# Kernel optimization log

Hardware: AMD Instinct MI355X
Metric: run time of the kernel (lower is better)

The kernel has to match this reference:

```python
import jax, jax.numpy as jnp
import numpy as np

N = 100_000          # ent_num
D = 256              # ent_dim
E_RAND = 3_200_000   # random edges (avg degree 32); + N self loops
NEG_SLOPE = 0.2      # LeakyReLU slope used by SpGraphAttentionLayer


def setup_inputs() -> dict:
    key = jax.random.key(0)
    k0, k1, k2, k3, k4, k5 = jax.random.split(key, 6)
    edges_rand = jax.random.randint(k0, (2, E_RAND), 0, N, dtype=jnp.int32)
    self_loops = jnp.tile(jnp.arange(N, dtype=jnp.int32)[None, :], (2, 1))
    edges = jnp.concatenate([edges_rand, self_loops], axis=1)  # [2, E]
    scale_w = 1.0 / np.sqrt(D).astype(np.float32)
    scale_a = 0.1 / np.sqrt(D).astype(np.float32)
    emb = jax.random.normal(k1, (N, D), jnp.float32)
    W1 = jax.random.normal(k2, (D, D), jnp.float32) * scale_w
    a1 = jax.random.normal(k3, (2 * D,), jnp.float32) * scale_a
    W2 = jax.random.normal(k4, (D, D), jnp.float32) * scale_w
    a2 = jax.random.normal(k5, (2 * D,), jnp.float32) * scale_a
    return {"emb": emb, "W1": W1, "a1": a1, "W2": W2, "a2": a2, "edges": edges}


def gat_layer(h, W, a, src, dst):
    # h: [N, D] node features; edges (src -> aggregates from dst)
    h2 = h @ W                              # [N, D]
    s_src = h2 @ a[:D]                      # [N] contribution of a . h_src
    s_dst = h2 @ a[D:]                      # [N] contribution of a . h_dst
    score = s_src[src] + s_dst[dst]         # [E] = a . [h_src; h_dst]
    e = jnp.exp(-jax.nn.leaky_relu(score, NEG_SLOPE))  # [E], pyGAT sparse form
    denom = jax.ops.segment_sum(e, src, num_segments=h.shape[0])          # [N]
    num = jax.ops.segment_sum(e[:, None] * h2[dst], src,
                              num_segments=h.shape[0])                    # [N, D]
    return jax.nn.elu(num / denom[:, None])


def reference(emb, W1, a1, W2, a2, edges):
    src, dst = edges[0], edges[1]
    h = gat_layer(emb, W1, a1, src, dst)
    h = gat_layer(h, W2, a2, src, dst)
    return h
```

## Files before the change

kernel.cpp:

```cpp
#include <hip/hip_runtime.h>
#include <hip/hip_bf16.h>

#define D 256
#define NEG_SLOPE 0.2f
#define BM 128
#define BN 128
#define BK 64
#define LDK 72
#define CAP 96

using bf16x8 = __attribute__((ext_vector_type(8))) __bf16;
using f32x4  = __attribute__((ext_vector_type(4))) float;
using u32x4  = __attribute__((ext_vector_type(4))) unsigned int;

__device__ __forceinline__ float bf2f(unsigned short u) {
    return __uint_as_float(((unsigned int)u) << 16);
}
__device__ __forceinline__ unsigned short f2bf(float f) {
    unsigned int u = __float_as_uint(f);
    unsigned int r = (u + 0x7FFF + ((u >> 16) & 1)) >> 16;
    return (unsigned short)r;
}


__global__ __launch_bounds__(256) void prep_kernel(
    const float* __restrict__ W1, const float* __restrict__ W2,
    unsigned short* __restrict__ WT1, unsigned short* __restrict__ WT2,
    int4* __restrict__ zbase, int nz16)
{
    const int b = blockIdx.x, tid = threadIdx.x;
    if (b < 256) {
        WT1[(size_t)tid * D + b] = f2bf(W1[(size_t)b * D + tid]);
    } else if (b < 512) {
        const int k = b - 256;
        WT2[(size_t)tid * D + k] = f2bf(W2[(size_t)k * D + tid]);
    } else {
        const int w = (b - 512) * 256 + tid;
        if (w < nz16) zbase[w] = make_int4(0, 0, 0, 0);
    }
}


__global__ void fill_kernel(const int* __restrict__ src, const int* __restrict__ dst,
                            int* __restrict__ fillp, int* __restrict__ col, int E) {
    int t = blockIdx.x * blockDim.x + threadIdx.x;
    if (t < E) {
        const int s = src[t];
        const int pos = atomicAdd(&fillp[s], 1);
        col[(size_t)s * CAP + pos] = dst[t];
    }
}


__global__ __launch_bounds__(256) void gemm_mfma(
    const unsigned short* __restrict__ Ab, const float* __restrict__ Af,
    const unsigned short* __restrict__ BT,
    unsigned short* __restrict__ C, int M,
    const float* __restrict__ av, float* __restrict__ s_src, float* __restrict__ s_dst)
{
    __shared__ unsigned short smem[2 * BM * LDK];
    unsigned short* As_ = smem;
    unsigned short* Bs_ = smem + BM * LDK;
    const int tid = threadIdx.x;
    const int m0 = blockIdx.x * BM;
    const int n0 = blockIdx.y * BN;
    const int lane = tid & 63;
    const int wv = tid >> 6;
    const int wm = (wv & 1) * 64;
    const int wn = (wv >> 1) * 64;
    const int l15 = lane & 15;
    const int quad = lane >> 4;

    f32x4 acc[4][4];
    #pragma unroll
    for (int i = 0; i < 4; ++i)
        #pragma unroll
        for (int j = 0; j < 4; ++j)
            acc[i][j] = (f32x4){0.f, 0.f, 0.f, 0.f};

    for (int k0 = 0; k0 < D; k0 += BK) {
        #pragma unroll
        for (int c = tid; c < BM * 8; c += 256) {
            const int row = c >> 3, j = c & 7;
            const int gr = m0 + row;
            uint4 avv = make_uint4(0, 0, 0, 0);
            if (gr < M) {
                if (Af) {
                    const float* p = Af + (size_t)gr * D + k0 + j * 8;
                    const float4 f0 = *(const float4*)p;
                    const float4 f1 = *(const float4*)(p + 4);
                    avv.x = (unsigned int)f2bf(f0.x) | ((unsigned int)f2bf(f0.y) << 16);
                    avv.y = (unsigned int)f2bf(f0.z) | ((unsigned int)f2bf(f0.w) << 16);
                    avv.z = (unsigned int)f2bf(f1.x) | ((unsigned int)f2bf(f1.y) << 16);
                    avv.w = (unsigned int)f2bf(f1.z) | ((unsigned int)f2bf(f1.w) << 16);
                } else {
                    avv = *(const uint4*)(Ab + (size_t)gr * D + k0 + j * 8);
                }
            }
            *(uint4*)(As_ + row * LDK + j * 8) = avv;
            const uint4 bv = *(const uint4*)(BT + (size_t)(n0 + row) * D + k0 + j * 8);
            *(uint4*)(Bs_ + row * LDK + j * 8) = bv;
        }
        __syncthreads();
        #pragma unroll
        for (int s = 0; s < 2; ++s) {
            bf16x8 af[4], bfr[4];
            #pragma unroll
            for (int i = 0; i < 4; ++i)
                af[i] = *(const bf16x8*)(As_ + (wm + i * 16 + l15) * LDK + s * 32 + quad * 8);
            #pragma unroll
            for (int j = 0; j < 4; ++j)
                bfr[j] = *(const bf16x8*)(Bs_ + (wn + j * 16 + l15) * LDK + s * 32 + quad * 8);
            #pragma unroll
            for (int i = 0; i < 4; ++i)
                #pragma unroll
                for (int j = 0; j < 4; ++j)
                    acc[i][j] = __builtin_amdgcn_mfma_f32_16x16x32_bf16(
                        af[i], bfr[j], acc[i][j], 0, 0, 0);
        }
        __syncthreads();
    }

    unsigned short* Cw = smem + wv * (64 * LDK);
    #pragma unroll
    for (int i = 0; i < 4; ++i)
        #pragma unroll
        for (int j = 0; j < 4; ++j)
            #pragma unroll
            for (int r = 0; r < 4; ++r)
                Cw[(i * 16 + quad * 4 + r) * LDK + j * 16 + l15] = f2bf(acc[i][j][r]);
    __syncthreads();
    const int ccol = n0 + wn + (lane & 31) * 2;
    const float a1c0 = av[ccol],     a1c1 = av[ccol + 1];
    const float a2c0 = av[D + ccol], a2c1 = av[D + ccol + 1];
    #pragma unroll
    for (int rr = 0; rr < 64; rr += 2) {
        const int row = rr + (lane >> 5);
        const unsigned int wd = *(const unsigned int*)(Cw + row * LDK + (lane & 31) * 2);
        const int gr = m0 + wm + row;
        if (gr < M)
            *(unsigned int*)(C + (size_t)gr * D + ccol) = wd;
        const float f0 = bf2f((unsigned short)(wd & 0xffffu));
        const float f1 = bf2f((unsigned short)(wd >> 16));
        float p1 = f0 * a1c0 + f1 * a1c1;
        float p2 = f0 * a2c0 + f1 * a2c1;
        #pragma unroll
        for (int off = 16; off > 0; off >>= 1) {
            p1 += __shfl_xor(p1, off);
            p2 += __shfl_xor(p2, off);
        }
        if ((lane & 31) == 0 && gr < M) {
            atomicAdd(&s_src[gr], p1);
            atomicAdd(&s_dst[gr], p2);
        }
    }
}


__global__ __launch_bounds__(256) void agg_kernel(
    const unsigned short* __restrict__ h2, const float* __restrict__ s_src,
    const float* __restrict__ s_dst, const int* __restrict__ deg,
    const int* __restrict__ col, unsigned short* __restrict__ out_bf16,
    float* __restrict__ out_f32, int Nn)
{
    const int lane = threadIdx.x & 63;
    const int half = lane >> 5;
    const int hl = lane & 31;
    const int node = blockIdx.x * 4 + (threadIdx.x >> 6);
    if (node >= Nn) return;
    const int total = deg[node];
    const int beg = node * CAP;
    const float ssrc = s_src[node];
    const unsigned short* hp = h2 + hl * 8;

    float a[8];
    #pragma unroll
    for (int i = 0; i < 8; ++i) a[i] = 0.f;
    float dpart = 0.f;

    for (int c0 = 0; c0 < total; c0 += 64) {
        const int cnt = min(64, total - c0);
        int j = 0;
        float e = 0.f;
        if (lane < cnt) {
            j = col[beg + c0 + lane];
            const float sc = ssrc + s_dst[j];
            const float l = sc >= 0.f ? sc : NEG_SLOPE * sc;
            e = __expf(-l);
        }
        dpart += e;
        for (int k = 0; k < cnt; k += 8) {
            const int   j0 = __shfl(j, k + 0 + half);
            const int   j1 = __shfl(j, k + 2 + half);
            const int   j2 = __shfl(j, k + 4 + half);
            const int   j3 = __shfl(j, k + 6 + half);
            const float e0 = __shfl(e, k + 0 + half);
            const float e1 = __shfl(e, k + 2 + half);
            const float e2 = __shfl(e, k + 4 + half);
            const float e3 = __shfl(e, k + 6 + half);
            const uint4 u0 = *(const uint4*)(hp + (size_t)j0 * D);
            const uint4 u1 = *(const uint4*)(hp + (size_t)j1 * D);
            const uint4 u2 = *(const uint4*)(hp + (size_t)j2 * D);
            const uint4 u3 = *(const uint4*)(hp + (size_t)j3 * D);
            #define ACC8(u, ev)                                               \
                a[0] = fmaf(ev, __uint_as_float((u).x << 16), a[0]);          \
                a[1] = fmaf(ev, __uint_as_float((u).x & 0xffff0000u), a[1]);  \
                a[2] = fmaf(ev, __uint_as_float((u).y << 16), a[2]);          \
                a[3] = fmaf(ev, __uint_as_float((u).y & 0xffff0000u), a[3]);  \
                a[4] = fmaf(ev, __uint_as_float((u).z << 16), a[4]);          \
                a[5] = fmaf(ev, __uint_as_float((u).z & 0xffff0000u), a[5]);  \
                a[6] = fmaf(ev, __uint_as_float((u).w << 16), a[6]);          \
                a[7] = fmaf(ev, __uint_as_float((u).w & 0xffff0000u), a[7]);
            ACC8(u0, e0)
            ACC8(u1, e1)
            ACC8(u2, e2)
            ACC8(u3, e3)
            #undef ACC8
        }
    }

    #pragma unroll
    for (int i = 0; i < 8; ++i) a[i] += __shfl_xor(a[i], 32);

    float denom = dpart;
    #pragma unroll
    for (int off = 32; off > 0; off >>= 1) denom += __shfl_xor(denom, off);
    const float inv = 1.f / denom;

    if (half == 0) {
        float v[8];
        #pragma unroll
        for (int i = 0; i < 8; ++i) {
            const float x = a[i] * inv;
            v[i] = x > 0.f ? x : expm1f(x);
        }
        if (out_bf16) {
            u32x4 o;
            o.x = (unsigned int)f2bf(v[0]) | ((unsigned int)f2bf(v[1]) << 16);
            o.y = (unsigned int)f2bf(v[2]) | ((unsigned int)f2bf(v[3]) << 16);
            o.z = (unsigned int)f2bf(v[4]) | ((unsigned int)f2bf(v[5]) << 16);
            o.w = (unsigned int)f2bf(v[6]) | ((unsigned int)f2bf(v[7]) << 16);
            __builtin_nontemporal_store(o, (u32x4*)(out_bf16 + (size_t)node * D + hl * 8));
        } else {
            float* p = out_f32 + (size_t)node * D + hl * 8;
            f32x4 o0 = {v[0], v[1], v[2], v[3]};
            f32x4 o1 = {v[4], v[5], v[6], v[7]};
            __builtin_nontemporal_store(o0, (f32x4*)p);
            __builtin_nontemporal_store(o1, (f32x4*)(p + 4));
        }
    }
}


static inline size_t align_up(size_t x, size_t a) { return (x + a - 1) & ~(a - 1); }

extern "C" void kernel_launch(void* const* d_in, const int* in_sizes, int n_in,
                              void* d_out, int out_size, void* d_ws, size_t ws_size,
                              hipStream_t stream)
{
    const float* emb = (const float*)d_in[0];
    const float* W1  = (const float*)d_in[1];
    const float* a1  = (const float*)d_in[2];
    const float* W2  = (const float*)d_in[3];
    const float* a2  = (const float*)d_in[4];
    const int* edges = (const int*)d_in[5];
    const int Nn = in_sizes[0] / D;
    const int E  = in_sizes[5] / 2;
    const int* src = edges;
    const int* dst = edges + E;

    size_t off = 0;
    char* base = (char*)d_ws;
    unsigned short* hA = (unsigned short*)(base + off);
    off = align_up(off + (size_t)Nn * D * sizeof(unsigned short), 256);
    unsigned short* hB = (unsigned short*)(base + off);
    off = align_up(off + (size_t)Nn * D * sizeof(unsigned short), 256);
    unsigned short* WT1 = (unsigned short*)(base + off);
    off = align_up(off + (size_t)D * D * sizeof(unsigned short), 256);
    unsigned short* WT2 = (unsigned short*)(base + off);
    off = align_up(off + (size_t)D * D * sizeof(unsigned short), 256);

    char* zstart = base + off;
    float* s1s = (float*)(base + off); off += (size_t)Nn * sizeof(float);
    float* s1d = (float*)(base + off); off += (size_t)Nn * sizeof(float);
    float* s2s = (float*)(base + off); off += (size_t)Nn * sizeof(float);
    float* s2d = (float*)(base + off); off += (size_t)Nn * sizeof(float);
    off = align_up(off, 256);
    int* fillp = (int*)(base + off);   off = align_up(off + (size_t)Nn * sizeof(int), 256);
    const size_t zbytes = (size_t)(base + off - zstart);
    const int nz16 = (int)(zbytes / 16);

    int* col = (int*)(base + off);
    off = align_up(off + (size_t)Nn * CAP * sizeof(int), 256);

    const int zblocks = (nz16 + 255) / 256;
    prep_kernel<<<512 + zblocks, 256, 0, stream>>>(W1, W2, WT1, WT2, (int4*)zstart, nz16);

    fill_kernel<<<(E + 255) / 256, 256, 0, stream>>>(src, dst, fillp, col, E);

    dim3 ggrid((Nn + BM - 1) / BM, D / BN);
    const int agrid = (Nn + 3) / 4;
    gemm_mfma<<<ggrid, 256, 0, stream>>>(nullptr, emb, WT1, hA, Nn, a1, s1s, s1d);
    agg_kernel<<<agrid, 256, 0, stream>>>(hA, s1s, s1d, fillp, col, hB, nullptr, Nn);
    gemm_mfma<<<ggrid, 256, 0, stream>>>(hB, nullptr, WT2, hA, Nn, a2, s2s, s2d);
    agg_kernel<<<agrid, 256, 0, stream>>>(hA, s2s, s2d, fillp, col, nullptr,
                                          (float*)d_out, Nn);
}
```

Measured before the change: 1.016 ms.

## Shard edge-bucket fill across eight sub-buckets to reduce atomic contention

The fill kernel now scatters each edge into one of eight shards, chosen by block index. Each shard keeps its own per-node counter and a 24-slot bucket, so atomics on the same source node are spread over separate counters. The aggregation kernel rebuilds each node's neighbor list from the eight shard counts with a prefix sum, then maps each lane's index back to a shard and offset. In exchange, the counter array to zero grows eightfold, column reads are split over eight regions, and per-edge index decode adds work in the hot aggregation loop.

```diff
diff --git a/kernel.cpp b/kernel.cpp
--- a/kernel.cpp
+++ b/kernel.cpp
@@ -7,7 +7,8 @@
 #define BN 128
 #define BK 64
 #define LDK 72
-#define CAP 96
+#define NSHARD 8
+#define SUB 24
 
 using bf16x8 = __attribute__((ext_vector_type(8))) __bf16;
 using f32x4  = __attribute__((ext_vector_type(4))) float;
@@ -42,12 +43,15 @@
 
 
 __global__ void fill_kernel(const int* __restrict__ src, const int* __restrict__ dst,
-                            int* __restrict__ fillp, int* __restrict__ col, int E) {
-    int t = blockIdx.x * blockDim.x + threadIdx.x;
+                            int* __restrict__ fillp8, int* __restrict__ col8,
+                            int E, int Nn) {
+    const int t = blockIdx.x * blockDim.x + threadIdx.x;
+    const int sh = blockIdx.x & (NSHARD - 1);
     if (t < E) {
         const int s = src[t];
-        const int pos = atomicAdd(&fillp[s], 1);
-        col[(size_t)s * CAP + pos] = dst[t];
+        const int idx = sh * Nn + s;
+        const int pos = atomicAdd(&fillp8[idx], 1);
+        col8[(size_t)idx * SUB + pos] = dst[t];
     }
 }
 
@@ -159,8 +163,8 @@
 
 __global__ __launch_bounds__(256) void agg_kernel(
     const unsigned short* __restrict__ h2, const float* __restrict__ s_src,
-    const float* __restrict__ s_dst, const int* __restrict__ deg,
-    const int* __restrict__ col, unsigned short* __restrict__ out_bf16,
+    const float* __restrict__ s_dst, const int* __restrict__ deg8,
+    const int* __restrict__ col8, unsigned short* __restrict__ out_bf16,
     float* __restrict__ out_f32, int Nn)
 {
     const int lane = threadIdx.x & 63;
@@ -168,8 +172,17 @@
     const int hl = lane & 31;
     const int node = blockIdx.x * 4 + (threadIdx.x >> 6);
     if (node >= Nn) return;
-    const int total = deg[node];
-    const int beg = node * CAP;
+
+    int dmy = 0;
+    if (lane < NSHARD) dmy = deg8[lane * Nn + node];
+    int pre[NSHARD + 1];
+    pre[0] = 0;
+    #pragma unroll
+    for (int sh = 0; sh < NSHARD; ++sh) pre[sh + 1] = pre[sh] + __shfl(dmy, sh);
+    const int total = pre[NSHARD];
+    const size_t shstride = (size_t)Nn * SUB;
+    const size_t nodeoff = (size_t)node * SUB;
+
     const float ssrc = s_src[node];
     const unsigned short* hp = h2 + hl * 8;
 
@@ -183,7 +196,14 @@
         int j = 0;
         float e = 0.f;
         if (lane < cnt) {
-            j = col[beg + c0 + lane];
+            const int idx = c0 + lane;
+            int sh = 0;
+            #pragma unroll
+            for (int x = 1; x < NSHARD; ++x) sh += (idx >= pre[x]);
+            int pb = pre[0];
+            #pragma unroll
+            for (int x = 1; x < NSHARD; ++x) pb = (sh >= x) ? pre[x] : pb;
+            j = col8[(size_t)sh * shstride + nodeoff + (idx - pb)];
             const float sc = ssrc + s_dst[j];
             const float l = sc >= 0.f ? sc : NEG_SLOPE * sc;
             e = __expf(-l);
@@ -286,23 +306,24 @@
     float* s2s = (float*)(base + off); off += (size_t)Nn * sizeof(float);
     float* s2d = (float*)(base + off); off += (size_t)Nn * sizeof(float);
     off = align_up(off, 256);
-    int* fillp = (int*)(base + off);   off = align_up(off + (size_t)Nn * sizeof(int), 256);
+    int* fillp8 = (int*)(base + off);
+    off = align_up(off + (size_t)NSHARD * Nn * sizeof(int), 256);
     const size_t zbytes = (size_t)(base + off - zstart);
     const int nz16 = (int)(zbytes / 16);
 
-    int* col = (int*)(base + off);
-    off = align_up(off + (size_t)Nn * CAP * sizeof(int), 256);
+    int* col8 = (int*)(base + off);
+    off = align_up(off + (size_t)NSHARD * Nn * SUB * sizeof(int), 256);
 
     const int zblocks = (nz16 + 255) / 256;
     prep_kernel<<<512 + zblocks, 256, 0, stream>>>(W1, W2, WT1, WT2, (int4*)zstart, nz16);
 
-    fill_kernel<<<(E + 255) / 256, 256, 0, stream>>>(src, dst, fillp, col, E);
+    fill_kernel<<<(E + 255) / 256, 256, 0, stream>>>(src, dst, fillp8, col8, E, Nn);
 
     dim3 ggrid((Nn + BM - 1) / BM, D / BN);
     const int agrid = (Nn + 3) / 4;
     gemm_mfma<<<ggrid, 256, 0, stream>>>(nullptr, emb, WT1, hA, Nn, a1, s1s, s1d);
-    agg_kernel<<<agrid, 256, 0, stream>>>(hA, s1s, s1d, fillp, col, hB, nullptr, Nn);
+    agg_kernel<<<agrid, 256, 0, stream>>>(hA, s1s, s1d, fillp8, col8, hB, nullptr, Nn);
     gemm_mfma<<<ggrid, 256, 0, stream>>>(hB, nullptr, WT2, hA, Nn, a2, s2s, s2d);
-    agg_kernel<<<agrid, 256, 0, stream>>>(hA, s2s, s2d, fillp, col, nullptr,
+    agg_kernel<<<agrid, 256, 0, stream>>>(hA, s2s, s2d, fillp8, col8, nullptr,
                                           (float*)d_out, Nn);
 }
```

Measured after the change: 1.072 ms. 1.06x slower.
